# Kernel optimization log

Hardware: AMD Instinct MI355X
Metric: run time of the kernel (lower is better)

Reference implementation:

```python
import jax, jax.numpy as jnp
import numpy as np


def _cumcount(idx):
    # idx: [U] int. cumcount[u] = number of u' < u with idx[u'] == idx[u].
    eq = idx[:, None] == idx[None, :]                 # [U, U]
    return jnp.sum(jnp.tril(eq), axis=-1) - 1         # [U]


def setup_inputs() -> dict:
    key = jax.random.key(0)
    ks = jax.random.split(key, 10)
    B, U, E, G = 4, 4096, 128, 64
    s = 1.0 / np.sqrt(E)
    return {
        "xc_off_grid": jax.random.uniform(ks[0], (B, U, 2), jnp.float32),
        "xc_on_grid": jax.random.uniform(ks[1], (B, G, G, 2), jnp.float32),
        "zc_off_grid": jax.random.normal(ks[2], (B, U, E), jnp.float32),
        "zc_on_grid": jax.random.normal(ks[3], (B, G, G, E), jnp.float32),
        "latents": jax.random.normal(ks[4], (G * G, E), jnp.float32),
        "fake_embedding": jax.random.normal(ks[5], (E,), jnp.float32),
        "Wq": jax.random.normal(ks[6], (E, E), jnp.float32) * s,
        "Wk": jax.random.normal(ks[7], (E, E), jnp.float32) * s,
        "Wv": jax.random.normal(ks[8], (E, E), jnp.float32) * s,
        "Wo": jax.random.normal(ks[9], (E, E), jnp.float32) * s,
        "ignore_on_grid": 0,
    }


def reference(xc_off_grid, xc_on_grid, zc_off_grid, zc_on_grid, latents,
              fake_embedding, Wq, Wk, Wv, Wo, ignore_on_grid):
    B, U, E = zc_off_grid.shape
    grid_shape = xc_on_grid.shape[1:-1]
    dx = xc_on_grid.shape[-1]
    xc_on = xc_on_grid.reshape(B, -1, dx)             # [B, S, dx]
    zc_on = zc_on_grid.reshape(B, -1, E)              # [B, S, E]
    S = xc_on.shape[1]

    # nearest grid cell per off-grid point (L1 distance argmin)
    dist = jnp.sum(jnp.abs(xc_off_grid[:, :, None, :] - xc_on[:, None, :, :]), axis=-1)  # [B,U,S]
    nearest_idx = jnp.argmin(dist, axis=2)            # [B, U]

    cumcount = jax.vmap(_cumcount)(nearest_idx)       # [B, U] slot within the patch
    b_idx = jnp.arange(B)[:, None]
    counts = jnp.zeros((B, S), jnp.int32).at[jnp.broadcast_to(b_idx, (B, U)), nearest_idx].add(1)
    M = int(counts.max()) + 1                          # max patch size (+1 for on-grid token)

    b_u = jnp.broadcast_to(b_idx, (B, U))
    # scatter off-grid tokens into padded per-cell patches (fake slots = 0, masked below)
    joint = jnp.zeros((B, S, M, E), zc_off_grid.dtype).at[b_u, nearest_idx, cumcount].set(zc_off_grid)
    valid = jnp.zeros((B, S, M), bool).at[b_u, nearest_idx, cumcount].set(True).at[:, :, -1].set(True)
    if ignore_on_grid:
        last = jnp.broadcast_to(fake_embedding, (B, S, E))
    else:
        last = zc_on
    joint = joint.at[:, :, -1].set(last)

    # masked multi-head cross attention, 1 query (latent) per grid cell
    H = 8
    dh = E // H
    kv = joint.reshape(B * S, M, E)
    q = jnp.broadcast_to(latents[None, :, None, :], (B, S, 1, E)).reshape(B * S, 1, E)
    qh = (q @ Wq).reshape(B * S, 1, H, dh)
    kh = (kv @ Wk).reshape(B * S, M, H, dh)
    vh = (kv @ Wv).reshape(B * S, M, H, dh)
    scores = jnp.einsum('bqhd,bkhd->bhqk', qh, kh) / np.sqrt(dh).astype(np.float32)
    mask = valid.reshape(B * S, 1, 1, M)
    scores = jnp.where(mask, scores, jnp.float32(-1e30))
    attn = jax.nn.softmax(scores, axis=-1)
    out = jnp.einsum('bhqk,bkhd->bqhd', attn, vh).reshape(B * S, 1, E) @ Wo
    zc = out.reshape(B, S, E)
    return zc.reshape((B,) + tuple(grid_shape) + (E,))
```

## Files before the change

kernel.cpp:

```cpp
#include <hip/hip_runtime.h>
#include <math.h>
#include <float.h>

#define E_DIM 128
typedef unsigned short ushort_t;
typedef __bf16 bf16x8 __attribute__((ext_vector_type(8)));
typedef float  f32x4  __attribute__((ext_vector_type(4)));

__device__ inline ushort_t f2bf(float f) {
    union { float f; unsigned int u; } x; x.f = f;
    unsigned int r = x.u + 0x7fffu + ((x.u >> 16) & 1u);
    return (ushort_t)(r >> 16);
}
__device__ inline float bf2f(unsigned int hi16) {
    union { unsigned int u; float f; } x; x.u = hi16 << 16;
    return x.f;
}
__device__ inline void lexmin(float& d, int& i, float d2, int i2) {
    if (d2 < d || (d2 == d && i2 < i)) { d = d2; i = i2; }
}

__device__ inline void stage_A_f32(char* AsmB, const float* abase, const float* fake,
                                   bool ign, int tid) {
#pragma unroll
    for (int i = 0; i < 8; ++i) {
        int f = (tid + i * 256) * 4;
        int r = f >> 7, c = f & 127;
        float4 v = *(const float4*)(ign ? (fake + c) : (abase + f));
        unsigned int lo = (unsigned int)f2bf(v.x) | ((unsigned int)f2bf(v.y) << 16);
        unsigned int hi = (unsigned int)f2bf(v.z) | ((unsigned int)f2bf(v.w) << 16);
        *(uint2*)(AsmB + r * 256 + ((c * 2) ^ ((r & 7) << 4))) = make_uint2(lo, hi);
    }
}

__device__ inline void stage_WT(char* WsmB, const ushort_t* Wt, int tid) {
#pragma unroll
    for (int i = 0; i < 8; ++i) {
        int gb = (tid + i * 256) * 16;
        int n = gb >> 8, cb = gb & 255;
        uint4 v = *(const uint4*)((const char*)Wt + gb);
        *(uint4*)(WsmB + n * 256 + (cb ^ ((n & 7) << 4))) = v;
    }
}

__device__ inline void mma_16x128(char* AsmB, char* WsmB, int wv, int lane, f32x4 acc[8]) {
    int l15 = lane & 15, kg = lane >> 4;
    int r = wv * 16 + l15;
#pragma unroll
    for (int kc = 0; kc < 4; ++kc) {
        int kb = (kc * 32 + kg * 8) * 2;
        bf16x8 a = *(const bf16x8*)(AsmB + r * 256 + (kb ^ ((r & 7) << 4)));
#pragma unroll
        for (int nf = 0; nf < 8; ++nf) {
            int n = nf * 16 + l15;
            bf16x8 b = *(const bf16x8*)(WsmB + n * 256 + (kb ^ ((n & 7) << 4)));
            acc[nf] = __builtin_amdgcn_mfma_f32_16x16x32_bf16(a, b, acc[nf], 0, 0, 0);
        }
    }
}

__device__ inline void mma_16x128_dual(char* AsmB, char* Wsm0B, char* Wsm1B,
                                       int wv, int lane, f32x4 acc0[8], f32x4 acc1[8]) {
    int l15 = lane & 15, kg = lane >> 4;
    int r = wv * 16 + l15;
#pragma unroll
    for (int kc = 0; kc < 4; ++kc) {
        int kb = (kc * 32 + kg * 8) * 2;
        bf16x8 a = *(const bf16x8*)(AsmB + r * 256 + (kb ^ ((r & 7) << 4)));
#pragma unroll
        for (int nf = 0; nf < 8; ++nf) {
            int n = nf * 16 + l15;
            int nb = (kb ^ ((n & 7) << 4));
            bf16x8 b0 = *(const bf16x8*)(Wsm0B + n * 256 + nb);
            acc0[nf] = __builtin_amdgcn_mfma_f32_16x16x32_bf16(a, b0, acc0[nf], 0, 0, 0);
            bf16x8 b1 = *(const bf16x8*)(Wsm1B + n * 256 + nb);
            acc1[nf] = __builtin_amdgcn_mfma_f32_16x16x32_bf16(a, b1, acc1[nf], 0, 0, 0);
        }
    }
}

__device__ inline void epi_bf16(ushort_t* C, int row0, int wv, int lane, f32x4 acc[8]) {
    int l15 = lane & 15, kg = lane >> 4;
    int rbase = row0 + wv * 16 + kg * 4;
#pragma unroll
    for (int rr = 0; rr < 4; ++rr) {
        ushort_t* dst = C + (size_t)(rbase + rr) * E_DIM + l15;
#pragma unroll
        for (int nf = 0; nf < 8; ++nf) dst[nf * 16] = f2bf(acc[nf][rr]);
    }
}

__device__ inline void epi_f32(float* C, int row0, int wv, int lane, f32x4 acc[8]) {
    int l15 = lane & 15, kg = lane >> 4;
    int rbase = row0 + wv * 16 + kg * 4;
#pragma unroll
    for (int rr = 0; rr < 4; ++rr) {
        float* dst = C + (size_t)(rbase + rr) * E_DIM + l15;
#pragma unroll
        for (int nf = 0; nf < 8; ++nf) dst[nf * 16] = acc[nf][rr];
    }
}

#define ZERO_ACC(a) do { _Pragma("unroll") for (int _i = 0; _i < 8; ++_i) \
    (a)[_i] = (f32x4){0.f, 0.f, 0.f, 0.f}; } while (0)

__global__ __launch_bounds__(256) void pre_kernel(
        const float* __restrict__ xc_off, const float* __restrict__ xc_on,
        const float* __restrict__ Wq, const float* __restrict__ Wk,
        const float* __restrict__ Wv, const float* __restrict__ Wo,
        ushort_t* __restrict__ WT, int* __restrict__ nearest, int U, int S, int B) {
    __shared__ __align__(16) char smraw[36928];
    const int NB = (U / 32) * B;
    int bid = blockIdx.x;
    int tid = threadIdx.x;
    if (bid >= NB) {
        int base = (bid - NB) * 1024 + tid;
#pragma unroll
        for (int j = 0; j < 4; ++j) {
            int idx = base + j * 256;
            int w = idx >> 14;
            int rem = idx & 16383;
            int k = rem >> 7, n = rem & 127;
            const float* src = (w == 0) ? Wq : (w == 1) ? Wk : (w == 2) ? Wv : Wo;
            WT[(size_t)w * 16384 + n * E_DIM + k] = f2bf(src[k * E_DIM + n]);
        }
        return;
    }
    float4* on = (float4*)smraw;
    float (*sh_d)[32] = (float(*)[32])(smraw + 32768);
    int   (*sh_i)[32] = (int(*)[32])(smraw + 34816);
    int tpb = U / 32;
    int b = bid / tpb;
    int xt = bid - b * tpb;
    const float4* onb = (const float4*)(xc_on + (size_t)b * S * 2);
    for (int i = tid; i < S / 2; i += 256) on[i] = onb[i];
    __syncthreads();
    int part = tid >> 4;
    int ug   = tid & 15;
    int u0 = xt * 32 + ug * 2;
    const float2* offb = (const float2*)(xc_off + (size_t)b * U * 2);
    float2 pA = offb[u0], pB = offb[u0 + 1];
    int h0 = part * (S / 32), h1 = h0 + (S / 32);
    float dA0 = FLT_MAX, dA1 = FLT_MAX, dB0 = FLT_MAX, dB1 = FLT_MAX;
    int iA0 = 0, iA1 = 0, iB0 = 0, iB1 = 0;
    for (int h = h0; h < h1; ++h) {
        float4 cc = on[h];
        int s = h * 2;
        float a0 = fabsf(pA.x - cc.x) + fabsf(pA.y - cc.y);
        float a1 = fabsf(pA.x - cc.z) + fabsf(pA.y - cc.w);
        float b0 = fabsf(pB.x - cc.x) + fabsf(pB.y - cc.y);
        float b1 = fabsf(pB.x - cc.z) + fabsf(pB.y - cc.w);
        if (a0 < dA0) { dA0 = a0; iA0 = s; }
        if (a1 < dA1) { dA1 = a1; iA1 = s + 1; }
        if (b0 < dB0) { dB0 = b0; iB0 = s; }
        if (b1 < dB1) { dB1 = b1; iB1 = s + 1; }
    }
    lexmin(dA0, iA0, dA1, iA1);
    lexmin(dB0, iB0, dB1, iB1);
    sh_d[part][ug * 2] = dA0;     sh_i[part][ug * 2] = iA0;
    sh_d[part][ug * 2 + 1] = dB0; sh_i[part][ug * 2 + 1] = iB0;
    __syncthreads();
    if (tid < 32) {
        float d = sh_d[0][tid]; int i = sh_i[0][tid];
#pragma unroll
        for (int pp = 1; pp < 16; ++pp) lexmin(d, i, sh_d[pp][tid], sh_i[pp][tid]);
        nearest[b * U + xt * 32 + tid] = i;
    }
}

__global__ __launch_bounds__(256) void proj_csr_kernel(
        const float* __restrict__ latents, const float* __restrict__ zc_off,
        const float* __restrict__ zc_on, const float* __restrict__ fake,
        const int* __restrict__ ignore, const ushort_t* __restrict__ WT,
        ushort_t* __restrict__ Qpre, ushort_t* __restrict__ Koff,
        ushort_t* __restrict__ Voff, ushort_t* __restrict__ Kon,
        ushort_t* __restrict__ Von,
        const int* __restrict__ nearest, int* __restrict__ offsets,
        int* __restrict__ tokens, int S, int U, int B) {
    __shared__ __align__(16) char sm[81920];
    const int BU = B * U;
    const int tid = threadIdx.x;

    if (blockIdx.x < (unsigned)B) {
        int b = blockIdx.x;
        int* cnt  = (int*)sm;
        int* part = (int*)(sm + S * 4);
        const int* nb = nearest + (size_t)b * U;
        for (int s = tid; s < S; s += 256) cnt[s] = 0;
        __syncthreads();
        for (int i = tid; i < U; i += 256) atomicAdd(&cnt[nb[i]], 1);
        __syncthreads();
        const int items = S / 256;
        int base = tid * items;
        int sum = 0;
        for (int i = 0; i < items; ++i) sum += cnt[base + i];
        part[tid] = sum;
        __syncthreads();
        for (int off = 1; off < 256; off <<= 1) {
            int v = (tid >= off) ? part[tid - off] : 0;
            __syncthreads();
            part[tid] += v;
            __syncthreads();
        }
        int run = b * U + ((tid == 0) ? 0 : part[tid - 1]);
        for (int i = 0; i < items; ++i) {
            int c = cnt[base + i];
            offsets[b * S + base + i] = run;
            cnt[base + i] = run;
            run += c;
        }
        if (b == B - 1 && tid == 255) offsets[B * S] = B * U;
        __syncthreads();
        for (int i = tid; i < U; i += 256) {
            int pos = atomicAdd(&cnt[nb[i]], 1);
            tokens[pos] = i;
        }
        return;
    }

    char* AsmB  = sm;
    char* Wsm0B = sm + 16384;
    char* Wsm1B = sm + 49152;
    const int lane = tid & 63, wv = tid >> 6;
    const int nQ = S / 64, nOff = BU / 64;
    int t = blockIdx.x - B;
    const ushort_t* WqT = WT;
    const ushort_t* WkT = WT + 16384;
    const ushort_t* WvT = WT + 32768;

    if (t < nQ) {
        int row0 = t * 64;
        stage_A_f32(AsmB, latents + (size_t)row0 * E_DIM, nullptr, false, tid);
        stage_WT(Wsm0B, WqT, tid);
        __syncthreads();
        f32x4 acc[8]; ZERO_ACC(acc);
        mma_16x128(AsmB, Wsm0B, wv, lane, acc);
        epi_bf16(Qpre, row0, wv, lane, acc);
        return;
    }
    bool offg = (t < nQ + nOff);
    int tt = offg ? (t - nQ) : (t - nQ - nOff);
    int row0 = tt * 64;
    const float* A = offg ? zc_off : zc_on;
    bool ign = (!offg) && (*ignore != 0);
    ushort_t* C0 = offg ? Koff : Kon;
    ushort_t* C1 = offg ? Voff : Von;
    stage_A_f32(AsmB, A + (size_t)row0 * E_DIM, fake, ign, tid);
    stage_WT(Wsm0B, WkT, tid);
    stage_WT(Wsm1B, WvT, tid);
    __syncthreads();
    f32x4 acc0[8], acc1[8]; ZERO_ACC(acc0); ZERO_ACC(acc1);
    mma_16x128_dual(AsmB, Wsm0B, Wsm1B, wv, lane, acc0, acc1);
    epi_bf16(C0, row0, wv, lane, acc0);
    epi_bf16(C1, row0, wv, lane, acc1);
}

__global__ __launch_bounds__(256) void attn_kernel(
        const ushort_t* __restrict__ Qpre,
        const ushort_t* __restrict__ Koff, const ushort_t* __restrict__ Voff,
        const ushort_t* __restrict__ Kon, const ushort_t* __restrict__ Von,
        const int* __restrict__ offsets, const int* __restrict__ tokens,
        ushort_t* __restrict__ AO, int S, int U) {
    int wv = threadIdx.x >> 6;
    int lane = threadIdx.x & 63;
    int c = blockIdx.x * 4 + wv;
    int b = c / S;
    int cl = c - b * S;

    unsigned int qw = ((const unsigned int*)(Qpre + (size_t)cl * E_DIM))[lane];
    float q0 = bf2f(qw & 0xffffu) * 0.25f;
    float q1 = bf2f(qw >> 16) * 0.25f;

    unsigned int kw = ((const unsigned int*)(Kon + (size_t)c * E_DIM))[lane];
    float pp = q0 * bf2f(kw & 0xffffu) + q1 * bf2f(kw >> 16);
    pp += __shfl_xor(pp, 4, 8);
    pp += __shfl_xor(pp, 2, 8);
    pp += __shfl_xor(pp, 1, 8);
    unsigned int vw = ((const unsigned int*)(Von + (size_t)c * E_DIM))[lane];
    float mm = pp, ll = 1.f;
    float o0 = bf2f(vw & 0xffffu), o1 = bf2f(vw >> 16);

    int beg = offsets[c], end = offsets[c + 1];
    for (int t = beg; t < end; ++t) {
        int u = tokens[t];
        size_t rr = ((size_t)b * U + u) * E_DIM;
        unsigned int kw2 = ((const unsigned int*)(Koff + rr))[lane];
        unsigned int vw2 = ((const unsigned int*)(Voff + rr))[lane];
        float p2 = q0 * bf2f(kw2 & 0xffffu) + q1 * bf2f(kw2 >> 16);
        p2 += __shfl_xor(p2, 4, 8);
        p2 += __shfl_xor(p2, 2, 8);
        p2 += __shfl_xor(p2, 1, 8);
        float v0 = bf2f(vw2 & 0xffffu), v1 = bf2f(vw2 >> 16);
        float nm = fmaxf(mm, p2);
        float f = __expf(mm - nm), w = __expf(p2 - nm);
        ll = ll * f + w;
        o0 = o0 * f + w * v0;
        o1 = o1 * f + w * v1;
        mm = nm;
    }
    float inv = 1.f / ll;
    ((unsigned int*)(AO + (size_t)c * E_DIM))[lane] =
        (unsigned int)f2bf(o0 * inv) | ((unsigned int)f2bf(o1 * inv) << 16);
}

__global__ __launch_bounds__(256) void gemmO_kernel(
        const ushort_t* __restrict__ AO, const ushort_t* __restrict__ WoT,
        float* __restrict__ out, int BS) {
    __shared__ __align__(16) char sm[49152];
    char* AsmB = sm;
    char* WsmB = sm + 16384;
    int tid = threadIdx.x, lane = tid & 63, wv = tid >> 6;
    int row0 = blockIdx.x * 64;
    const char* abase = (const char*)(AO + (size_t)row0 * E_DIM);
#pragma unroll
    for (int i = 0; i < 4; ++i) {
        int gb = (tid + i * 256) * 16;
        int r = gb >> 8, cb = gb & 255;
        uint4 v = *(const uint4*)(abase + gb);
        *(uint4*)(AsmB + r * 256 + (cb ^ ((r & 7) << 4))) = v;
    }
    stage_WT(WsmB, WoT, tid);
    __syncthreads();
    f32x4 acc[8]; ZERO_ACC(acc);
    mma_16x128(AsmB, WsmB, wv, lane, acc);
    epi_f32(out, row0, wv, lane, acc);
}

extern "C" void kernel_launch(void* const* d_in, const int* in_sizes, int n_in,
                              void* d_out, int out_size, void* d_ws, size_t ws_size,
                              hipStream_t stream) {
    const float* xc_off  = (const float*)d_in[0];
    const float* xc_on   = (const float*)d_in[1];
    const float* zc_off  = (const float*)d_in[2];
    const float* zc_on   = (const float*)d_in[3];
    const float* latents = (const float*)d_in[4];
    const float* fake    = (const float*)d_in[5];
    const float* Wq      = (const float*)d_in[6];
    const float* Wk      = (const float*)d_in[7];
    const float* Wv      = (const float*)d_in[8];
    const float* Wo      = (const float*)d_in[9];
    const int*   ignore  = (const int*)d_in[10];

    const int E = in_sizes[5];
    const int S = in_sizes[4] / E;
    const int B = in_sizes[1] / (S * 2);
    const int U = in_sizes[0] / (B * 2);
    const int BS = B * S, BU = B * U;

    char* ws = (char*)d_ws;
    size_t off = 0;
    auto alloc = [&](size_t bytes) {
        size_t r = off;
        off += (bytes + 255) & ~(size_t)255;
        return r;
    };
    ushort_t* WT      = (ushort_t*)(ws + alloc((size_t)4 * E * E * 2));
    int*      nearest = (int*)(ws + alloc((size_t)BU * 4));
    int*      offsets = (int*)(ws + alloc((size_t)(BS + 1) * 4));
    int*      tokens  = (int*)(ws + alloc((size_t)BU * 4));
    ushort_t* Qpre    = (ushort_t*)(ws + alloc((size_t)S * E * 2));
    ushort_t* Koff    = (ushort_t*)(ws + alloc((size_t)BU * E * 2));
    ushort_t* Voff    = (ushort_t*)(ws + alloc((size_t)BU * E * 2));
    ushort_t* Kon     = (ushort_t*)(ws + alloc((size_t)BS * E * 2));
    ushort_t* Von     = (ushort_t*)(ws + alloc((size_t)BS * E * 2));
    ushort_t* AO      = (ushort_t*)(ws + alloc((size_t)BS * E * 2));

    const int NB = (U / 32) * B;
    pre_kernel<<<NB + 64, 256, 0, stream>>>(xc_off, xc_on, Wq, Wk, Wv, Wo,
                                            WT, nearest, U, S, B);

    const int ntile = S / 64 + BU / 64 + BS / 64;
    proj_csr_kernel<<<ntile + B, 256, 0, stream>>>(latents, zc_off, zc_on, fake, ignore,
                                                   WT, Qpre, Koff, Voff, Kon, Von,
                                                   nearest, offsets, tokens, S, U, B);

    attn_kernel<<<BS / 4, 256, 0, stream>>>(Qpre, Koff, Voff, Kon, Von,
                                            offsets, tokens, AO, S, U);

    gemmO_kernel<<<BS / 64, 256, 0, stream>>>(AO, WT + 3 * E * E, (float*)d_out, BS);
}
```

Before: 136.4 us.

## Fuse attention and output projection into one kernel via shared memory

Merges the per-cell attention kernel and the Wo GEMM into one kernel. Each 512-thread block computes attention for 64 cells, with 8 waves handling 8 rows each, and writes the bf16 results into swizzled LDS. The same block then runs MFMA against Wo staged in LDS, with each wave covering half of the output columns. This removes the AO global round trip and one kernel launch, at the cost of fewer blocks (BS/64 instead of BS/4) and less parallelism during the attention phase.

```diff
diff --git a/kernel.cpp b/kernel.cpp
--- a/kernel.cpp
+++ b/kernel.cpp
@@ -87,17 +87,6 @@
         ushort_t* dst = C + (size_t)(rbase + rr) * E_DIM + l15;
 #pragma unroll
         for (int nf = 0; nf < 8; ++nf) dst[nf * 16] = f2bf(acc[nf][rr]);
-    }
-}
-
-__device__ inline void epi_f32(float* C, int row0, int wv, int lane, f32x4 acc[8]) {
-    int l15 = lane & 15, kg = lane >> 4;
-    int rbase = row0 + wv * 16 + kg * 4;
-#pragma unroll
-    for (int rr = 0; rr < 4; ++rr) {
-        float* dst = C + (size_t)(rbase + rr) * E_DIM + l15;
-#pragma unroll
-        for (int nf = 0; nf < 8; ++nf) dst[nf * 16] = acc[nf][rr];
     }
 }
 
@@ -255,75 +244,93 @@
     epi_bf16(C1, row0, wv, lane, acc1);
 }
 
-__global__ __launch_bounds__(256) void attn_kernel(
+__global__ __launch_bounds__(512) void attn_gemmO_kernel(
         const ushort_t* __restrict__ Qpre,
         const ushort_t* __restrict__ Koff, const ushort_t* __restrict__ Voff,
         const ushort_t* __restrict__ Kon, const ushort_t* __restrict__ Von,
         const int* __restrict__ offsets, const int* __restrict__ tokens,
-        ushort_t* __restrict__ AO, int S, int U) {
-    int wv = threadIdx.x >> 6;
-    int lane = threadIdx.x & 63;
-    int c = blockIdx.x * 4 + wv;
-    int b = c / S;
-    int cl = c - b * S;
-
-    unsigned int qw = ((const unsigned int*)(Qpre + (size_t)cl * E_DIM))[lane];
-    float q0 = bf2f(qw & 0xffffu) * 0.25f;
-    float q1 = bf2f(qw >> 16) * 0.25f;
-
-    unsigned int kw = ((const unsigned int*)(Kon + (size_t)c * E_DIM))[lane];
-    float pp = q0 * bf2f(kw & 0xffffu) + q1 * bf2f(kw >> 16);
-    pp += __shfl_xor(pp, 4, 8);
-    pp += __shfl_xor(pp, 2, 8);
-    pp += __shfl_xor(pp, 1, 8);
-    unsigned int vw = ((const unsigned int*)(Von + (size_t)c * E_DIM))[lane];
-    float mm = pp, ll = 1.f;
-    float o0 = bf2f(vw & 0xffffu), o1 = bf2f(vw >> 16);
-
-    int beg = offsets[c], end = offsets[c + 1];
-    for (int t = beg; t < end; ++t) {
-        int u = tokens[t];
-        size_t rr = ((size_t)b * U + u) * E_DIM;
-        unsigned int kw2 = ((const unsigned int*)(Koff + rr))[lane];
-        unsigned int vw2 = ((const unsigned int*)(Voff + rr))[lane];
-        float p2 = q0 * bf2f(kw2 & 0xffffu) + q1 * bf2f(kw2 >> 16);
-        p2 += __shfl_xor(p2, 4, 8);
-        p2 += __shfl_xor(p2, 2, 8);
-        p2 += __shfl_xor(p2, 1, 8);
-        float v0 = bf2f(vw2 & 0xffffu), v1 = bf2f(vw2 >> 16);
-        float nm = fmaxf(mm, p2);
-        float f = __expf(mm - nm), w = __expf(p2 - nm);
-        ll = ll * f + w;
-        o0 = o0 * f + w * v0;
-        o1 = o1 * f + w * v1;
-        mm = nm;
-    }
-    float inv = 1.f / ll;
-    ((unsigned int*)(AO + (size_t)c * E_DIM))[lane] =
-        (unsigned int)f2bf(o0 * inv) | ((unsigned int)f2bf(o1 * inv) << 16);
-}
-
-__global__ __launch_bounds__(256) void gemmO_kernel(
-        const ushort_t* __restrict__ AO, const ushort_t* __restrict__ WoT,
-        float* __restrict__ out, int BS) {
+        const ushort_t* __restrict__ WoT, float* __restrict__ out, int S, int U) {
     __shared__ __align__(16) char sm[49152];
     char* AsmB = sm;
     char* WsmB = sm + 16384;
-    int tid = threadIdx.x, lane = tid & 63, wv = tid >> 6;
-    int row0 = blockIdx.x * 64;
-    const char* abase = (const char*)(AO + (size_t)row0 * E_DIM);
+    const int tid = threadIdx.x;
+    const int w = tid >> 6;
+    const int lane = tid & 63;
+    const int row0 = blockIdx.x * 64;
+
 #pragma unroll
     for (int i = 0; i < 4; ++i) {
-        int gb = (tid + i * 256) * 16;
-        int r = gb >> 8, cb = gb & 255;
-        uint4 v = *(const uint4*)(abase + gb);
-        *(uint4*)(AsmB + r * 256 + (cb ^ ((r & 7) << 4))) = v;
-    }
-    stage_WT(WsmB, WoT, tid);
+        int gb = (tid + i * 512) * 16;
+        int n = gb >> 8, cb = gb & 255;
+        uint4 v = *(const uint4*)((const char*)WoT + gb);
+        *(uint4*)(WsmB + n * 256 + (cb ^ ((n & 7) << 4))) = v;
+    }
+
+    for (int i = 0; i < 8; ++i) {
+        int r = w * 8 + i;
+        int c = row0 + r;
+        int b = c / S;
+        int cl = c - b * S;
+        unsigned int qw = ((const unsigned int*)(Qpre + (size_t)cl * E_DIM))[lane];
+        float q0 = bf2f(qw & 0xffffu) * 0.25f;
+        float q1 = bf2f(qw >> 16) * 0.25f;
+        unsigned int kw = ((const unsigned int*)(Kon + (size_t)c * E_DIM))[lane];
+        float pp = q0 * bf2f(kw & 0xffffu) + q1 * bf2f(kw >> 16);
+        pp += __shfl_xor(pp, 4, 8);
+        pp += __shfl_xor(pp, 2, 8);
+        pp += __shfl_xor(pp, 1, 8);
+        unsigned int vw = ((const unsigned int*)(Von + (size_t)c * E_DIM))[lane];
+        float mm = pp, ll = 1.f;
+        float o0 = bf2f(vw & 0xffffu), o1 = bf2f(vw >> 16);
+        int beg = offsets[c], end = offsets[c + 1];
+        for (int t = beg; t < end; ++t) {
+            int u = tokens[t];
+            size_t rr = ((size_t)b * U + u) * E_DIM;
+            unsigned int kw2 = ((const unsigned int*)(Koff + rr))[lane];
+            unsigned int vw2 = ((const unsigned int*)(Voff + rr))[lane];
+            float p2 = q0 * bf2f(kw2 & 0xffffu) + q1 * bf2f(kw2 >> 16);
+            p2 += __shfl_xor(p2, 4, 8);
+            p2 += __shfl_xor(p2, 2, 8);
+            p2 += __shfl_xor(p2, 1, 8);
+            float v0 = bf2f(vw2 & 0xffffu), v1 = bf2f(vw2 >> 16);
+            float nm = fmaxf(mm, p2);
+            float f = __expf(mm - nm), wgt = __expf(p2 - nm);
+            ll = ll * f + wgt;
+            o0 = o0 * f + wgt * v0;
+            o1 = o1 * f + wgt * v1;
+            mm = nm;
+        }
+        float inv = 1.f / ll;
+        unsigned int res = (unsigned int)f2bf(o0 * inv) | ((unsigned int)f2bf(o1 * inv) << 16);
+        *(unsigned int*)(AsmB + r * 256 + ((4 * lane) ^ ((r & 7) << 4))) = res;
+    }
     __syncthreads();
-    f32x4 acc[8]; ZERO_ACC(acc);
-    mma_16x128(AsmB, WsmB, wv, lane, acc);
-    epi_f32(out, row0, wv, lane, acc);
+
+    const int wvr = w & 3;
+    const int nh = w >> 2;
+    const int l15 = lane & 15, kg = lane >> 4;
+    f32x4 acc[4];
+#pragma unroll
+    for (int j = 0; j < 4; ++j) acc[j] = (f32x4){0.f, 0.f, 0.f, 0.f};
+    int r = wvr * 16 + l15;
+#pragma unroll
+    for (int kc = 0; kc < 4; ++kc) {
+        int kb = (kc * 32 + kg * 8) * 2;
+        bf16x8 a = *(const bf16x8*)(AsmB + r * 256 + (kb ^ ((r & 7) << 4)));
+#pragma unroll
+        for (int j = 0; j < 4; ++j) {
+            int n = (nh * 4 + j) * 16 + l15;
+            bf16x8 b = *(const bf16x8*)(WsmB + n * 256 + (kb ^ ((n & 7) << 4)));
+            acc[j] = __builtin_amdgcn_mfma_f32_16x16x32_bf16(a, b, acc[j], 0, 0, 0);
+        }
+    }
+    int rbase = row0 + wvr * 16 + kg * 4;
+#pragma unroll
+    for (int rr = 0; rr < 4; ++rr) {
+        float* dst = out + (size_t)(rbase + rr) * E_DIM + nh * 64 + l15;
+#pragma unroll
+        for (int j = 0; j < 4; ++j) dst[j * 16] = acc[j][rr];
+    }
 }
 
 extern "C" void kernel_launch(void* const* d_in, const int* in_sizes, int n_in,
@@ -363,7 +370,6 @@
     ushort_t* Voff    = (ushort_t*)(ws + alloc((size_t)BU * E * 2));
     ushort_t* Kon     = (ushort_t*)(ws + alloc((size_t)BS * E * 2));
     ushort_t* Von     = (ushort_t*)(ws + alloc((size_t)BS * E * 2));
-    ushort_t* AO      = (ushort_t*)(ws + alloc((size_t)BS * E * 2));
 
     const int NB = (U / 32) * B;
     pre_kernel<<<NB + 64, 256, 0, stream>>>(xc_off, xc_on, Wq, Wk, Wv, Wo,
@@ -374,8 +380,7 @@
                                                    WT, Qpre, Koff, Voff, Kon, Von,
                                                    nearest, offsets, tokens, S, U, B);
 
-    attn_kernel<<<BS / 4, 256, 0, stream>>>(Qpre, Koff, Voff, Kon, Von,
-                                            offsets, tokens, AO, S, U);
-
-    gemmO_kernel<<<BS / 64, 256, 0, stream>>>(AO, WT + 3 * E * E, (float*)d_out, BS);
-}
+    attn_gemmO_kernel<<<BS / 64, 512, 0, stream>>>(Qpre, Koff, Voff, Kon, Von,
+                                                   offsets, tokens, WT + 3 * E * E,
+                                                   (float*)d_out, S, U);
+}
```

After: 141.7 us. 1.04x slower.
